# Optimization experiments

Hardware: AMD Instinct MI355X
Metric: run time of the kernel (lower is better)

Reference implementation:

```python
import jax, jax.numpy as jnp
import numpy as np

N = 49152       # nodes
EH = 8192       # hyperedges (star nodes)
M = N + EH
F = 256         # num_features == expan_dim == MLP_hidden
D = 256
HEADS = 8
CHUNK = 1024
NE_N = 10 * N   # nnz of N x N sparse mats
NE_M = 10 * M   # nnz of M x M sparse mats


def spmm(row, col, val, X, n):
    # sparse [n, m] (COO) @ dense X [m, d] -> [n, d]
    return jax.ops.segment_sum(val[:, None] * X[col], row, num_segments=n)


def expan_net(x, row, col, val, Ws, bs, n):
    # 2-layer GCN: (A @ (X @ W) + b), ReLU between; dropout is identity in eval.
    h = spmm(row, col, val, x @ Ws[0], n) + bs[0]
    h = jax.nn.relu(h)
    return spmm(row, col, val, h @ Ws[1], n) + bs[1]


def chunked_mha(q, k, v, in_w, in_b, out_w, out_b):
    # torch nn.MultiheadAttention on unbatched [L, D] chunks of size CHUNK
    n, d = q.shape
    c = n // CHUNK
    dh = d // HEADS
    wq, wk, wv = jnp.split(in_w, 3, axis=0)
    bq, bk, bv = jnp.split(in_b, 3)
    def resh(t):
        return t.reshape(c, CHUNK, HEADS, dh)
    qh = resh(q @ wq.T + bq)
    kh = resh(k @ wk.T + bk)
    vh = resh(v @ wv.T + bv)
    scale = 1.0 / np.sqrt(dh)
    scores = jnp.einsum('clhe,cmhe->chlm', qh, kh) * scale  # [c,H,CHUNK,CHUNK]
    attn = jax.nn.softmax(scores, axis=-1)
    out = jnp.einsum('chlm,cmhe->clhe', attn, vh).reshape(n, d)
    return out @ out_w.T + out_b


def setup_inputs():
    key = jax.random.key(0)
    ks = iter(jax.random.split(key, 64))
    nrm = lambda shape, s=1.0: jax.random.normal(next(ks), shape, dtype=jnp.float32) * s
    uni = lambda shape: jax.random.uniform(next(ks), shape, dtype=jnp.float32)
    ridx = lambda shape, hi: jax.random.randint(next(ks), shape, 0, hi, dtype=jnp.int32)
    inp = {'x': nrm((N, F))}
    for nm, ne, hi in [('A_cg', NE_N, N), ('A_hyp', NE_N, N), ('A_sg', NE_M, M),
                       ('L_cg', NE_N, N), ('L_hyp', NE_N, N), ('L_sg', NE_M, M)]:
        inp[nm + '_row'] = ridx((ne,), hi)
        inp[nm + '_col'] = ridx((ne,), hi)
        inp[nm + '_val'] = uni((ne,)) * 0.1
    for p in ['cg', 'hg', 'sg']:
        inp[p + '_W'] = nrm((2, F, D), 0.05)
        inp[p + '_b'] = nrm((2, D), 0.05)
    for p in ['sn_hyp', 'sn_cg', 'sn_sg']:
        inp[p + '_W'] = nrm((D, D), 0.05)
        inp[p + '_b'] = nrm((D,), 0.05)
    for p in ['spa', 'spe']:
        for q in ['hyp', 'star', 'clq']:
            inp[f'{p}_{q}_W'] = nrm((D, D), 0.05)
            inp[f'{p}_{q}_b'] = nrm((D,), 0.05)
        inp[p + '_in_w'] = nrm((3 * D, D), 0.05)
        inp[p + '_in_b'] = nrm((3 * D,), 0.05)
        inp[p + '_out_w'] = nrm((D, D), 0.05)
        inp[p + '_out_b'] = nrm((D,), 0.05)
    return inp


def reference(x,
              A_cg_row, A_cg_col, A_cg_val, A_hyp_row, A_hyp_col, A_hyp_val,
              A_sg_row, A_sg_col, A_sg_val, L_cg_row, L_cg_col, L_cg_val,
              L_hyp_row, L_hyp_col, L_hyp_val, L_sg_row, L_sg_col, L_sg_val,
              cg_W, cg_b, hg_W, hg_b, sg_W, sg_b,
              sn_hyp_W, sn_hyp_b, sn_cg_W, sn_cg_b, sn_sg_W, sn_sg_b,
              spa_hyp_W, spa_hyp_b, spa_star_W, spa_star_b, spa_clq_W, spa_clq_b,
              spa_in_w, spa_in_b, spa_out_w, spa_out_b,
              spe_hyp_W, spe_hyp_b, spe_star_W, spe_star_b, spe_clq_W, spe_clq_b,
              spe_in_w, spe_in_b, spe_out_w, spe_out_b):
    n = x.shape[0]
    # star features: nodes first, zero-init hyperedge rows (v_mask == [True]*N+[False]*EH)
    x_star = jnp.concatenate([x, jnp.zeros((EH, x.shape[1]), x.dtype)], axis=0)
    # 1. Expansion graph convolutions
    cg_feat = expan_net(x, A_cg_row, A_cg_col, A_cg_val, cg_W, cg_b, n)
    hg_feat = expan_net(x, A_hyp_row, A_hyp_col, A_hyp_val, hg_W, hg_b, n)
    sg_feat = expan_net(x_star, A_sg_row, A_sg_col, A_sg_val, sg_W, sg_b, n + EH)
    X_star, S_star = sg_feat[:n], sg_feat[n:]
    # 2. SmoothNet: linear then Laplacian spmm
    X_hyp = spmm(L_hyp_row, L_hyp_col, L_hyp_val, hg_feat @ sn_hyp_W.T + sn_hyp_b, n)
    X_cg = spmm(L_cg_row, L_cg_col, L_cg_val, cg_feat @ sn_cg_W.T + sn_cg_b, n)
    X_sg = spmm(L_sg_row, L_sg_col, L_sg_val, sg_feat @ sn_sg_W.T + sn_sg_b, n + EH)
    # 3. TAA attention (chunked MHA, Q/K/V = hyp/star/clique projections)
    X_spectral = chunked_mha(X_hyp @ spe_hyp_W.T + spe_hyp_b,
                             X_cg @ spe_star_W.T + spe_star_b,
                             X_sg[:n] @ spe_clq_W.T + spe_clq_b,
                             spe_in_w, spe_in_b, spe_out_w, spe_out_b)
    X_spatial = chunked_mha(hg_feat @ spa_hyp_W.T + spa_hyp_b,
                            cg_feat @ spa_star_W.T + spa_star_b,
                            X_star @ spa_clq_W.T + spa_clq_b,
                            spa_in_w, spa_in_b, spa_out_w, spa_out_b)
    taa = jnp.concatenate([X_spatial, X_spectral], axis=1)
    return taa, X_star, S_star
```

## Files before the change

kernel.cpp:

```cpp
#include <hip/hip_runtime.h>

#define NN 49152
#define EHN 8192
#define MM (NN + EHN)
#define FD 256
#define DD 256
#define NHEADS 8
#define DHEAD 32
#define CHK 1024
#define NEN (10 * NN)
#define NEM (10 * MM)
#define ROWS_TOT (4 * NN + 2 * MM)
#define ETOT (4 * NEN + 2 * NEM)

typedef __bf16 bf16x8 __attribute__((ext_vector_type(8)));
typedef unsigned short u16x8 __attribute__((ext_vector_type(8)));
typedef float f32x4 __attribute__((ext_vector_type(4)));

static __device__ __forceinline__ unsigned short f2bf(float f) {
  unsigned int u = __float_as_uint(f);
  unsigned int r = (u + 0x7FFFu + ((u >> 16) & 1u)) >> 16;
  return (unsigned short)r;
}
static __device__ __forceinline__ float bf2f(unsigned short u) {
  return __uint_as_float((unsigned int)u << 16);
}
static __device__ __forceinline__ unsigned int cvtpk(float a, float b) {
  unsigned int r;
  asm("v_cvt_pk_bf16_f32 %0, %1, %2" : "=v"(r) : "v"(a), "v"(b));
  return r;
}
static __device__ __forceinline__ float max3f(float a, float b, float c) {
  return fmaxf(fmaxf(a, b), c);
}

struct CastJobs {
  const float* src[8];
  unsigned short* dst[8];
  int trans[8];
};
__global__ __launch_bounds__(256) void cast_w8_kernel(CastJobs jobs)
{
  int job = blockIdx.x >> 8;
  int i = (blockIdx.x & 255) * 256 + threadIdx.x;
  int n = i >> 8, k = i & 255;
  const float* src = jobs.src[job];
  float f = jobs.trans[job] ? src[(size_t)k * 256 + n] : src[i];
  jobs.dst[job][i] = f2bf(f);
}

__global__ __launch_bounds__(256) void combine_w_kernel(
    const float* __restrict__ Bw, const float* __restrict__ Aw,
    const float* __restrict__ ab, const float* __restrict__ bb,
    unsigned short* __restrict__ Wc, float* __restrict__ bc, float fscale)
{
  int n = blockIdx.x, t = threadIdx.x;
  __shared__ float shB[256];
  __shared__ float red[256];
  shB[t] = Bw[n * 256 + t];
  __syncthreads();
  float acc = 0.0f;
  #pragma unroll 8
  for (int j = 0; j < 256; ++j) acc += shB[j] * Aw[j * 256 + t];
  Wc[n * 256 + t] = f2bf(acc * fscale);
  red[t] = shB[t] * ab[t];
  __syncthreads();
  for (int off = 128; off; off >>= 1) {
    if (t < off) red[t] += red[t + off];
    __syncthreads();
  }
  if (t == 0) bc[n] = (red[0] + bb[n]) * fscale;
}

__global__ __launch_bounds__(256) void mm256f_kernel(
    const float* __restrict__ A, const float* __restrict__ B,
    float* __restrict__ C)
{
  int n = blockIdx.x, t = threadIdx.x;
  __shared__ float sa[256];
  sa[t] = A[n * 256 + t];
  __syncthreads();
  float acc = 0.0f;
  #pragma unroll 8
  for (int j = 0; j < 256; ++j) acc += sa[j] * B[j * 256 + t];
  C[n * 256 + t] = acc;
}

__global__ __launch_bounds__(256) void mm256b_kernel(
    const float* __restrict__ A, const float* __restrict__ B,
    unsigned short* __restrict__ W, float fs)
{
  int n = blockIdx.x, t = threadIdx.x;
  __shared__ float sa[256];
  sa[t] = A[n * 256 + t];
  __syncthreads();
  float acc = 0.0f;
  #pragma unroll 8
  for (int j = 0; j < 256; ++j) acc += sa[j] * B[j * 256 + t];
  W[n * 256 + t] = f2bf(acc * fs);
}

__global__ __launch_bounds__(256) void mv256_kernel(
    const float* __restrict__ W, const float* __restrict__ v,
    const float* __restrict__ add, float* __restrict__ outv, float fs)
{
  int t = threadIdx.x;
  __shared__ float sv[256];
  sv[t] = v[t];
  __syncthreads();
  float acc = 0.0f;
  #pragma unroll 8
  for (int k = 0; k < 256; ++k) acc += W[t * 256 + k] * sv[k];
  if (add) acc += add[t];
  outv[t] = fs * acc;
}

struct Gemm3 {
  const void* A[3];
  const unsigned short* W[3];
  const float* c0[3];
  const float* rs[3];
  const float* cvec[3];
  unsigned short* out[3];
  int bs1, bs2, btot;
};
template<int ABF>
__global__ __launch_bounds__(256) void gemm3_kernel(Gemm3 g)
{
  const int b = blockIdx.x;
  const int j = (b >= g.bs2) ? 2 : (b >= g.bs1 ? 1 : 0);
  const int bm = (b - (j == 2 ? g.bs2 : j == 1 ? g.bs1 : 0)) * 64;
  const void* Ain = g.A[j];
  const unsigned short* Wt = g.W[j];

  __shared__ __align__(16) char sA[2][4096];
  __shared__ __align__(16) char sB[2][16384];
  const int tid = threadIdx.x, lane = tid & 63, wid = tid >> 6;
  const int l15 = lane & 15, l4 = lane >> 4;

  f32x4 acc[16] = {};
  const int ar = tid >> 2, akq = (tid & 3) * 8;
  const int bn = tid;

  float4 fa0, fa1;
  u16x8 ua;
  u16x8 rb0, rb1, rb2, rb3;
  auto stage_load = [&](int k0) {
    if (ABF) {
      ua = *(const u16x8*)((const unsigned short*)Ain +
                           (size_t)(bm + ar) * 256 + k0 + akq);
    } else {
      const float* ap = (const float*)Ain + (size_t)(bm + ar) * 256 + k0 + akq;
      fa0 = *(const float4*)ap;
      fa1 = *(const float4*)(ap + 4);
    }
    const unsigned short* bp = Wt + (size_t)bn * 256 + k0;
    rb0 = *(const u16x8*)bp;        rb1 = *(const u16x8*)(bp + 8);
    rb2 = *(const u16x8*)(bp + 16); rb3 = *(const u16x8*)(bp + 24);
  };
  auto stage_write = [&](int buf) {
    u16x8 va;
    if (ABF) {
      va = ua;
    } else {
      va[0] = f2bf(fa0.x); va[1] = f2bf(fa0.y); va[2] = f2bf(fa0.z); va[3] = f2bf(fa0.w);
      va[4] = f2bf(fa1.x); va[5] = f2bf(fa1.y); va[6] = f2bf(fa1.z); va[7] = f2bf(fa1.w);
    }
    int aa = ((ar << 6) + (akq << 1)) ^ ((ar & 7) << 4);
    *(u16x8*)(sA[buf] + aa) = va;
    int bb = (bn << 6) ^ ((bn & 7) << 4);
    *(u16x8*)(sB[buf] + bb) = rb0;
    *(u16x8*)(sB[buf] + (bb ^ 16)) = rb1;
    *(u16x8*)(sB[buf] + (bb ^ 32)) = rb2;
    *(u16x8*)(sB[buf] + (bb ^ 48)) = rb3;
  };

  stage_load(0);
  stage_write(0);
  __syncthreads();
  int cur = 0;
  for (int it = 0; it < 8; ++it) {
    if (it < 7) stage_load((it + 1) * 32);
    int ra = wid * 16 + l15;
    bf16x8 af = *(const bf16x8*)(sA[cur] + ((ra << 6) + (l4 << 4) ^ ((ra & 7) << 4)));
    #pragma unroll
    for (int n4 = 0; n4 < 16; ++n4) {
      int rn = n4 * 16 + l15;
      bf16x8 bf = *(const bf16x8*)(sB[cur] + ((rn << 6) + (l4 << 4) ^ ((rn & 7) << 4)));
      acc[n4] = __builtin_amdgcn_mfma_f32_16x16x32_bf16(af, bf, acc[n4], 0, 0, 0);
    }
    __syncthreads();
    if (it < 7) {
      stage_write(cur ^ 1);
      __syncthreads();
      cur ^= 1;
    }
  }
  const int row = bm + wid * 16 + l4 * 4;
  const float* rs = g.rs[j];
  const float* c0 = g.c0[j];
  const float* cvec = g.cvec[j];
  unsigned short* Cout = g.out[j];
  float rsv[4];
  if (rs) {
    #pragma unroll
    for (int jj = 0; jj < 4; ++jj) rsv[jj] = rs[row + jj];
  }
  #pragma unroll
  for (int n4 = 0; n4 < 16; ++n4) {
    int col = n4 * 16 + l15;
    float base = c0 ? c0[col] : 0.0f;
    float cv = rs ? cvec[col] : 0.0f;
    #pragma unroll
    for (int jj = 0; jj < 4; ++jj) {
      float v = acc[n4][jj] + base;
      if (rs) v += rsv[jj] * cv;
      Cout[(size_t)(row + jj) * 256 + col] = f2bf(v);
    }
  }
}

__global__ __launch_bounds__(256) void gemmout2_kernel(
    const unsigned short* __restrict__ A0, const unsigned short* __restrict__ W0,
    const float* __restrict__ b0,
    const unsigned short* __restrict__ A1, const unsigned short* __restrict__ W1,
    const float* __restrict__ b1,
    float* __restrict__ Cout)
{
  const int job = blockIdx.x >= (NN / 64);
  const int bm = (blockIdx.x - (job ? NN / 64 : 0)) * 64;
  const unsigned short* Ain = job ? A1 : A0;
  const unsigned short* Wt  = job ? W1 : W0;
  const float* c0 = job ? b1 : b0;
  const int coff = job ? 0 : 256;

  __shared__ __align__(16) char sA[2][4096];
  __shared__ __align__(16) char sB[2][16384];
  const int tid = threadIdx.x, lane = tid & 63, wid = tid >> 6;
  const int l15 = lane & 15, l4 = lane >> 4;

  f32x4 acc[16] = {};
  const int ar = tid >> 2, akq = (tid & 3) * 8;
  const int bn = tid;
  u16x8 ua, rb0, rb1, rb2, rb3;
  auto stage_load = [&](int k0) {
    ua = *(const u16x8*)(Ain + (size_t)(bm + ar) * 256 + k0 + akq);
    const unsigned short* bp = Wt + (size_t)bn * 256 + k0;
    rb0 = *(const u16x8*)bp;        rb1 = *(const u16x8*)(bp + 8);
    rb2 = *(const u16x8*)(bp + 16); rb3 = *(const u16x8*)(bp + 24);
  };
  auto stage_write = [&](int buf) {
    int aa = ((ar << 6) + (akq << 1)) ^ ((ar & 7) << 4);
    *(u16x8*)(sA[buf] + aa) = ua;
    int bb = (bn << 6) ^ ((bn & 7) << 4);
    *(u16x8*)(sB[buf] + bb) = rb0;
    *(u16x8*)(sB[buf] + (bb ^ 16)) = rb1;
    *(u16x8*)(sB[buf] + (bb ^ 32)) = rb2;
    *(u16x8*)(sB[buf] + (bb ^ 48)) = rb3;
  };
  stage_load(0);
  stage_write(0);
  __syncthreads();
  int cur = 0;
  for (int it = 0; it < 8; ++it) {
    if (it < 7) stage_load((it + 1) * 32);
    int ra = wid * 16 + l15;
    bf16x8 af = *(const bf16x8*)(sA[cur] + ((ra << 6) + (l4 << 4) ^ ((ra & 7) << 4)));
    #pragma unroll
    for (int n4 = 0; n4 < 16; ++n4) {
      int rn = n4 * 16 + l15;
      bf16x8 bf = *(const bf16x8*)(sB[cur] + ((rn << 6) + (l4 << 4) ^ ((rn & 7) << 4)));
      acc[n4] = __builtin_amdgcn_mfma_f32_16x16x32_bf16(af, bf, acc[n4], 0, 0, 0);
    }
    __syncthreads();
    if (it < 7) {
      stage_write(cur ^ 1);
      __syncthreads();
      cur ^= 1;
    }
  }
  const int row = bm + wid * 16 + l4 * 4;
  #pragma unroll
  for (int n4 = 0; n4 < 16; ++n4) {
    int col = n4 * 16 + l15;
    float base = c0[col];
    #pragma unroll
    for (int jj = 0; jj < 4; ++jj)
      Cout[(size_t)(row + jj) * 512 + coff + col] = acc[n4][jj] + base;
  }
}

struct CooPtrs {
  const int* rw[6];
  const int* cl[6];
  const float* vl[6];
};
static __device__ __forceinline__ void coo_block_resolve(
    int b, int& g, int& eb, int& rb)
{
  if      (b < 1920) { g = 0; eb = 0;    rb = 0; }
  else if (b < 3840) { g = 1; eb = 1920; rb = NN; }
  else if (b < 6080) { g = 2; eb = 3840; rb = 2 * NN; }
  else if (b < 8000) { g = 3; eb = 6080; rb = 2 * NN + MM; }
  else if (b < 9920) { g = 4; eb = 8000; rb = 3 * NN + MM; }
  else               { g = 5; eb = 9920; rb = 4 * NN + MM; }
}

__global__ __launch_bounds__(256) void count_all_kernel(
    CooPtrs coo, int* __restrict__ cnt)
{
  int g, eb, rb;
  coo_block_resolve(blockIdx.x, g, eb, rb);
  int e = (blockIdx.x - eb) * 256 + threadIdx.x;
  atomicAdd(&cnt[rb + coo.rw[g][e]], 1);
}

__global__ __launch_bounds__(256) void scan1_kernel(
    const int* __restrict__ cnt, int* __restrict__ bsum, int n)
{
  __shared__ int sh[256];
  int i = blockIdx.x * 256 + threadIdx.x;
  sh[threadIdx.x] = (i < n) ? cnt[i] : 0;
  __syncthreads();
  for (int off = 128; off; off >>= 1) {
    if (threadIdx.x < off) sh[threadIdx.x] += sh[threadIdx.x + off];
    __syncthreads();
  }
  if (threadIdx.x == 0) bsum[blockIdx.x] = sh[0];
}

__global__ __launch_bounds__(256) void scan2_kernel(int* __restrict__ bsum, int nb)
{
  __shared__ int sh[256];
  int t = threadIdx.x;
  int carry = 0;
  for (int base = 0; base < nb; base += 256) {
    int i = base + t;
    int v = (i < nb) ? bsum[i] : 0;
    sh[t] = v;
    __syncthreads();
    for (int off = 1; off < 256; off <<= 1) {
      int add = (t >= off) ? sh[t - off] : 0;
      __syncthreads();
      sh[t] += add;
      __syncthreads();
    }
    int incl = sh[t];
    int tot = sh[255];
    if (i < nb) bsum[i] = carry + incl - v;
    carry += tot;
    __syncthreads();
  }
}

__global__ __launch_bounds__(256) void scan3_kernel(
    const int* __restrict__ cnt, const int* __restrict__ bsum,
    int* __restrict__ rowptr, int* __restrict__ cntz, int n)
{
  __shared__ int sh[256];
  int i = blockIdx.x * 256 + threadIdx.x;
  int v = (i < n) ? cnt[i] : 0;
  sh[threadIdx.x] = v;
  __syncthreads();
  for (int off = 1; off < 256; off <<= 1) {
    int add = (threadIdx.x >= off) ? sh[threadIdx.x - off] : 0;
    __syncthreads();
    sh[threadIdx.x] += add;
    __syncthreads();
  }
  int incl = sh[threadIdx.x];
  int base = bsum[blockIdx.x];
  if (i < n) { rowptr[i] = base + incl - v; cntz[i] = 0; }
  if (i == n - 1) rowptr[n] = base + incl;
}

__global__ __launch_bounds__(256) void fill_all_kernel(
    CooPtrs coo, const int* __restrict__ P, int* __restrict__ cur,
    int2* __restrict__ epack)
{
  int g, eb, rb;
  coo_block_resolve(blockIdx.x, g, eb, rb);
  int e = (blockIdx.x - eb) * 256 + threadIdx.x;
  int grow = rb + coo.rw[g][e];
  int pos = P[grow] + atomicAdd(&cur[grow], 1);
  epack[pos] = make_int2(coo.cl[g][e], __float_as_int(coo.vl[g][e]));
}

__global__ __launch_bounds__(256) void rowsum_all_kernel(
    const int* __restrict__ P, const int2* __restrict__ epack,
    float* __restrict__ rsAll)
{
  int j = blockIdx.x * 256 + threadIdx.x;
  int g = j / NN;
  int r = j - g * NN;
  int grow = (g == 0 ? 2 * NN + MM : g == 1 ? 3 * NN + MM : 4 * NN + MM) + r;
  float s = 0.0f;
  int end = P[grow + 1];
  for (int e = P[grow]; e < end; ++e) s += __int_as_float(epack[e].y);
  rsAll[j] = s;
}

struct Spmm3 {
  const int* rowptr[3];
  const unsigned short* X[3];
  unsigned short* Y[3];
  float* Y2[3];
  const float* bias[3];
  int src_rows[3];
  int bs1, bs2;
};
__global__ __launch_bounds__(256) void spmm3_kernel(
    Spmm3 s, const int2* __restrict__ ep, int relu)
{
  const int b = blockIdx.x;
  const int j = (b >= s.bs2) ? 2 : (b >= s.bs1 ? 1 : 0);
  const int rblk = b - (j == 2 ? s.bs2 : j == 1 ? s.bs1 : 0);
  const int wave = threadIdx.x >> 6, lane = threadIdx.x & 63;
  const int r = rblk * 4 + wave;
  const int f0 = lane * 4;
  const int src_rows = s.src_rows[j];
  const unsigned short* X = s.X[j];
  const int* rowptr = s.rowptr[j];
  int e = rowptr[r], end = rowptr[r + 1];
  float a0 = 0.0f, a1 = 0.0f, a2 = 0.0f, a3 = 0.0f;
  for (; e + 3 < end; e += 4) {
    int2 cv0 = ep[e], cv1 = ep[e + 1], cv2 = ep[e + 2], cv3 = ep[e + 3];
    ushort4 x0 = {0,0,0,0}, x1 = {0,0,0,0}, x2 = {0,0,0,0}, x3 = {0,0,0,0};
    if (cv0.x < src_rows) x0 = *(const ushort4*)(X + (size_t)cv0.x * DD + f0);
    if (cv1.x < src_rows) x1 = *(const ushort4*)(X + (size_t)cv1.x * DD + f0);
    if (cv2.x < src_rows) x2 = *(const ushort4*)(X + (size_t)cv2.x * DD + f0);
    if (cv3.x < src_rows) x3 = *(const ushort4*)(X + (size_t)cv3.x * DD + f0);
    float v0 = __int_as_float(cv0.y), v1 = __int_as_float(cv1.y);
    float v2 = __int_as_float(cv2.y), v3 = __int_as_float(cv3.y);
    if (cv0.x < src_rows) { a0 += v0*bf2f(x0.x); a1 += v0*bf2f(x0.y); a2 += v0*bf2f(x0.z); a3 += v0*bf2f(x0.w); }
    if (cv1.x < src_rows) { a0 += v1*bf2f(x1.x); a1 += v1*bf2f(x1.y); a2 += v1*bf2f(x1.z); a3 += v1*bf2f(x1.w); }
    if (cv2.x < src_rows) { a0 += v2*bf2f(x2.x); a1 += v2*bf2f(x2.y); a2 += v2*bf2f(x2.z); a3 += v2*bf2f(x2.w); }
    if (cv3.x < src_rows) { a0 += v3*bf2f(x3.x); a1 += v3*bf2f(x3.y); a2 += v3*bf2f(x3.z); a3 += v3*bf2f(x3.w); }
  }
  for (; e < end; ++e) {
    int2 cv = ep[e];
    if (cv.x < src_rows) {
      float v = __int_as_float(cv.y);
      ushort4 xx = *(const ushort4*)(X + (size_t)cv.x * DD + f0);
      a0 += v * bf2f(xx.x); a1 += v * bf2f(xx.y);
      a2 += v * bf2f(xx.z); a3 += v * bf2f(xx.w);
    }
  }
  const float* bias = s.bias[j];
  if (bias) {
    a0 += bias[f0]; a1 += bias[f0 + 1]; a2 += bias[f0 + 2]; a3 += bias[f0 + 3];
  }
  if (relu) {
    a0 = fmaxf(a0, 0.0f); a1 = fmaxf(a1, 0.0f);
    a2 = fmaxf(a2, 0.0f); a3 = fmaxf(a3, 0.0f);
  }
  uint2 yb = { cvtpk(a0, a1), cvtpk(a2, a3) };
  *(uint2*)(s.Y[j] + (size_t)r * DD + f0) = yb;
  if (s.Y2[j]) {
    float4 yf = {a0, a1, a2, a3};
    *(float4*)(s.Y2[j] + (size_t)r * DD + f0) = yf;
  }
}

__global__ __launch_bounds__(256) void attn2_kernel(
    const unsigned short* __restrict__ Q1, const unsigned short* __restrict__ K1,
    const unsigned short* __restrict__ V1, unsigned short* __restrict__ O1,
    const unsigned short* __restrict__ Q2, const unsigned short* __restrict__ K2,
    const unsigned short* __restrict__ V2, unsigned short* __restrict__ O2)
{
  __shared__ __align__(16) char sKb[4096];
  __shared__ __align__(16) char sVb[4096];
  __shared__ __align__(16) char sPb[8192];
  const int wgid = (blockIdx.x & 7) * 1536 + (blockIdx.x >> 3);
  const int qb = wgid & 15, h = (wgid >> 4) & 7, cc = wgid >> 7;
  const int job = cc >= 48;
  const int c = cc - (job ? 48 : 0);
  const unsigned short* Q = job ? Q2 : Q1;
  const unsigned short* K = job ? K2 : K1;
  const unsigned short* V = job ? V2 : V1;
  unsigned short* O = job ? O2 : O1;

  const int tid = threadIdx.x, lane = tid & 63, wid = tid >> 6;
  const int l15 = lane & 15, l4 = lane >> 4;
  char* sPw = sPb + wid * 2048;
  const size_t base = (size_t)c * (CHK * DD) + (size_t)h * DHEAD;
  const int q0 = qb * 64 + wid * 16;

  bf16x8 qf = *(const bf16x8*)(Q + base + (size_t)(q0 + l15) * DD + l4 * 8);

  const int key_s = tid >> 2, dq = (tid & 3) * 8;
  const unsigned short* Kp = K + base + (size_t)key_s * DD + dq;
  const unsigned short* Vp = V + base + (size_t)key_s * DD + dq;
  const int kaddr = ((key_s << 6) + (dq << 1)) ^ ((key_s & 7) << 4);

  f32x4 oacc[2] = {};
  float m = -1e30f, l = 0.0f;
  const f32x4 zero = {};

  for (int kt = 0; kt < CHK; kt += 64) {
    __syncthreads();
    u16x8 kv = *(const u16x8*)Kp;  Kp += 64 * DD;
    u16x8 vv = *(const u16x8*)Vp;  Vp += 64 * DD;
    *(u16x8*)(sKb + kaddr) = kv;
    #pragma unroll
    for (int i = 0; i < 8; ++i) {
      int d = dq + i;
      int bb = ((d << 7) + (key_s << 1))
             ^ ((d & 7) << 4) ^ (((d >> 3) & 3) << 5);
      *(unsigned short*)(sVb + bb) = vv[i];
    }
    __syncthreads();

    f32x4 s[4];
    #pragma unroll
    for (int s4 = 0; s4 < 4; ++s4) {
      int key = s4 * 16 + l15;
      int ba = ((key << 6) + (l4 << 4)) ^ ((key & 7) << 4);
      bf16x8 kf = *(const bf16x8*)(sKb + ba);
      s[s4] = __builtin_amdgcn_mfma_f32_16x16x32_bf16(kf, qf, zero, 0, 0, 0);
    }
    float t0 = max3f(s[0][0], s[0][1], s[0][2]);
    float t1 = max3f(s[0][3], s[1][0], s[1][1]);
    float t2 = max3f(s[1][2], s[1][3], s[2][0]);
    float t3 = max3f(s[2][1], s[2][2], s[2][3]);
    float t4 = max3f(s[3][0], s[3][1], s[3][2]);
    float tmax = max3f(max3f(t0, t1, t2), fmaxf(t3, t4), s[3][3]);
    tmax = fmaxf(tmax, __shfl_xor(tmax, 16));
    tmax = fmaxf(tmax, __shfl_xor(tmax, 32));
    bool skip = __all(tmax - m <= 8.0f);
    float mnew = skip ? m : fmaxf(m, tmax);
    if (!skip) {
      float corr = __builtin_amdgcn_exp2f(m - mnew);
      l *= corr;
      oacc[0] *= corr;
      oacc[1] *= corr;
    }
    float psum = 0.0f;
    float p[4][4];
    #pragma unroll
    for (int s4 = 0; s4 < 4; ++s4)
      #pragma unroll
      for (int j = 0; j < 4; ++j) {
        p[s4][j] = __builtin_amdgcn_exp2f(s[s4][j] - mnew);
        psum += p[s4][j];
      }
    psum += __shfl_xor(psum, 16);
    psum += __shfl_xor(psum, 32);
    l += psum;
    m = mnew;
    #pragma unroll
    for (int s4 = 0; s4 < 4; ++s4) {
      uint2 pk = { cvtpk(p[s4][0], p[s4][1]), cvtpk(p[s4][2], p[s4][3]) };
      int bp = ((l15 << 7) + (s4 << 5) + (l4 << 3)) ^ ((l15 & 3) << 5);
      *(uint2*)(sPw + bp) = pk;
    }
    __syncthreads();

    #pragma unroll
    for (int dh = 0; dh < 2; ++dh)
      #pragma unroll
      for (int kh = 0; kh < 2; ++kh) {
        int d = dh * 16 + l15;
        int ba = ((d << 7) + ((kh * 32 + l4 * 8) << 1))
               ^ ((d & 7) << 4) ^ (((d >> 3) & 3) << 5);
        bf16x8 vf = *(const bf16x8*)(sVb + ba);
        int bp = ((l15 << 7) + (kh << 6) + (l4 << 4)) ^ ((l15 & 3) << 5);
        bf16x8 pf = *(const bf16x8*)(sPw + bp);
        oacc[dh] = __builtin_amdgcn_mfma_f32_16x16x32_bf16(vf, pf, oacc[dh], 0, 0, 0);
      }
  }

  float inv = 1.0f / l;
  unsigned short* orow = O + base + (size_t)(q0 + l15) * DD;
  #pragma unroll
  for (int dh = 0; dh < 2; ++dh) {
    uint2 o2 = { cvtpk(oacc[dh][0] * inv, oacc[dh][1] * inv),
                 cvtpk(oacc[dh][2] * inv, oacc[dh][3] * inv) };
    *(uint2*)(orow + dh * 16 + l4 * 4) = o2;
  }
}

__global__ __launch_bounds__(256) void fill_kernel(float* p, long n, float v)
{
  long i = (long)blockIdx.x * 256 + threadIdx.x;
  if (i < n) p[i] = v;
}

extern "C" void kernel_launch(void* const* d_in, const int* in_sizes, int n_in,
                              void* d_out, int out_size, void* d_ws, size_t ws_size,
                              hipStream_t stream)
{
  const float* x     = (const float*)d_in[0];
  const int*   Acg_r = (const int*)d_in[1];
  const int*   Acg_c = (const int*)d_in[2];
  const float* Acg_v = (const float*)d_in[3];
  const int*   Ahy_r = (const int*)d_in[4];
  const int*   Ahy_c = (const int*)d_in[5];
  const float* Ahy_v = (const float*)d_in[6];
  const int*   Asg_r = (const int*)d_in[7];
  const int*   Asg_c = (const int*)d_in[8];
  const float* Asg_v = (const float*)d_in[9];
  const int*   Lcg_r = (const int*)d_in[10];
  const int*   Lcg_c = (const int*)d_in[11];
  const float* Lcg_v = (const float*)d_in[12];
  const int*   Lhy_r = (const int*)d_in[13];
  const int*   Lhy_c = (const int*)d_in[14];
  const float* Lhy_v = (const float*)d_in[15];
  const int*   Lsg_r = (const int*)d_in[16];
  const int*   Lsg_c = (const int*)d_in[17];
  const float* Lsg_v = (const float*)d_in[18];
  const float* cg_W  = (const float*)d_in[19];
  const float* cg_b  = (const float*)d_in[20];
  const float* hg_W  = (const float*)d_in[21];
  const float* hg_b  = (const float*)d_in[22];
  const float* sg_W  = (const float*)d_in[23];
  const float* sg_b  = (const float*)d_in[24];
  const float* snh_W = (const float*)d_in[25];
  const float* snh_b = (const float*)d_in[26];
  const float* snc_W = (const float*)d_in[27];
  const float* snc_b = (const float*)d_in[28];
  const float* sns_W = (const float*)d_in[29];
  const float* sns_b = (const float*)d_in[30];
  const float* spa_hyp_W  = (const float*)d_in[31];
  const float* spa_hyp_b  = (const float*)d_in[32];
  const float* spa_star_W = (const float*)d_in[33];
  const float* spa_star_b = (const float*)d_in[34];
  const float* spa_clq_W  = (const float*)d_in[35];
  const float* spa_clq_b  = (const float*)d_in[36];
  const float* spa_in_w   = (const float*)d_in[37];
  const float* spa_in_b   = (const float*)d_in[38];
  const float* spa_out_w  = (const float*)d_in[39];
  const float* spa_out_b  = (const float*)d_in[40];
  const float* spe_hyp_W  = (const float*)d_in[41];
  const float* spe_hyp_b  = (const float*)d_in[42];
  const float* spe_star_W = (const float*)d_in[43];
  const float* spe_star_b = (const float*)d_in[44];
  const float* spe_clq_W  = (const float*)d_in[45];
  const float* spe_clq_b  = (const float*)d_in[46];
  const float* spe_in_w   = (const float*)d_in[47];
  const float* spe_in_b   = (const float*)d_in[48];
  const float* spe_out_w  = (const float*)d_in[49];
  const float* spe_out_b  = (const float*)d_in[50];

  float* out = (float*)d_out;

  const size_t NF = (size_t)NN * DD;
  const size_t MF = (size_t)MM * DD;
  const size_t WELEMS  = 14u * 65536u;
  const size_t need = (14 * NF + 3 * MF) * 2
                    + (size_t)ETOT * 8
                    + ((size_t)3 * NN + 65536 + 256 + 4096) * 4
                    + ((size_t)ROWS_TOT + 1 + ROWS_TOT + 2048) * 4
                    + WELEMS * 2;

  auto fill = [&](float v) {
    long tot = (long)out_size;
    fill_kernel<<<dim3((unsigned)((tot + 255) / 256)), 256, 0, stream>>>(out, tot, v);
  };
  if (ws_size < need)                        { fill(12.0f); return; }
  if (n_in != 51)                            { fill(16.0f); return; }
  if (in_sizes[0] != NN * FD)                { fill(20.0f); return; }
  if (in_sizes[3] != NEN)                    { fill(24.0f); return; }
  if (in_sizes[9] != NEM)                    { fill(28.0f); return; }
  if (in_sizes[19] != 2 * FD * DD)           { fill(32.0f); return; }
  if (in_sizes[37] != 3 * DD * DD)           { fill(36.0f); return; }
  if (out_size != NN * 512 + NN * DD + EHN * DD) { fill(40.0f); return; }

  unsigned short* Tcg = (unsigned short*)d_ws;
  unsigned short* Thy = Tcg + NF;
  unsigned short* Tsg = Thy + NF;
  unsigned short* Hcg = Tsg + NF;
  unsigned short* Hhy = Hcg + NF;
  unsigned short* Hsg = Hhy + NF;
  unsigned short* Usg = Hsg + MF;
  unsigned short* SG  = Usg + MF;
  unsigned short* CG  = SG + MF;
  unsigned short* HG  = CG + NF;
  unsigned short* LH  = HG + NF;
  unsigned short* LC  = LH + NF;
  unsigned short* LS  = LC + NF;
  unsigned short* QH  = LS + NF;
  unsigned short* KH  = QH + NF;
  unsigned short* VH  = KH + NF;
  unsigned short* AOx = VH + NF;
  unsigned short* Ucg = Tcg;
  unsigned short* Uhy = Thy;
  unsigned short* Q2  = LH;
  unsigned short* K2  = LC;
  unsigned short* V2  = LS;
  unsigned short* AO1 = Hcg;
  unsigned short* AO2 = Hhy;
  (void)AOx;

  int2* epack = (int2*)(AOx + NF);
  float* fp = (float*)(epack + ETOT);
  float* rsAll = fp;           fp += 3 * NN;
  float* tmp256 = fp;          fp += 65536;
  float* tmpv = fp;            fp += 256;
  float* CB = fp;              fp += 4096;
  int* P    = (int*)fp;
  int* cnt  = P + ROWS_TOT + 1;
  int* bsum = cnt + ROWS_TOT;
  unsigned short* WB = (unsigned short*)(bsum + 2048);

  int* rp_cg  = P;
  int* rp_hy  = P + NN;
  int* rp_sg  = P + 2 * NN;
  int* rp_Lcg = P + 2 * NN + MM;
  int* rp_Lhy = P + 3 * NN + MM;
  int* rp_Lsg = P + 4 * NN + MM;
  float* rs_c = rsAll;
  float* rs_h = rsAll + NN;
  float* rs_s = rsAll + 2 * NN;

  auto wslot = [&](int s) { return WB + (size_t)s * 65536; };
  auto cb    = [&](int s) { return CB + (size_t)s * 256; };

  auto combine = [&](const float* Bw, const float* Aw, const float* ab,
                     const float* bb, unsigned short* Wc, float* bcp, float fs) {
    combine_w_kernel<<<dim3(256), 256, 0, stream>>>(Bw, Aw, ab, bb, Wc, bcp, fs);
  };
  auto combine3 = [&](const float* w3, const float* b3, const float* pW,
                      const float* pb, const float* sW, const float* sb,
                      unsigned short* Wc, float* cvecp, float* c0p, float fs) {
    mm256f_kernel<<<dim3(256), 256, 0, stream>>>(pW, sW, tmp256);
    mm256b_kernel<<<dim3(256), 256, 0, stream>>>(w3, tmp256, Wc, fs);
    mv256_kernel<<<dim3(1), 256, 0, stream>>>(pW, sb, nullptr, tmpv, 1.0f);
    mv256_kernel<<<dim3(1), 256, 0, stream>>>(w3, tmpv, nullptr, cvecp, fs);
    mv256_kernel<<<dim3(1), 256, 0, stream>>>(w3, pb, b3, c0p, fs);
  };

  const float fsQ = 0.17677669529663687f * 1.4426950408889634f;

  {
    CastJobs jobs;
    jobs.src[0] = cg_W;           jobs.dst[0] = wslot(0);  jobs.trans[0] = 1;
    jobs.src[1] = cg_W + FD * DD; jobs.dst[1] = wslot(1);  jobs.trans[1] = 1;
    jobs.src[2] = hg_W;           jobs.dst[2] = wslot(2);  jobs.trans[2] = 1;
    jobs.src[3] = hg_W + FD * DD; jobs.dst[3] = wslot(3);  jobs.trans[3] = 1;
    jobs.src[4] = sg_W;           jobs.dst[4] = wslot(4);  jobs.trans[4] = 1;
    jobs.src[5] = sg_W + FD * DD; jobs.dst[5] = wslot(5);  jobs.trans[5] = 1;
    jobs.src[6] = spa_out_w;      jobs.dst[6] = wslot(12); jobs.trans[6] = 0;
    jobs.src[7] = spe_out_w;      jobs.dst[7] = wslot(13); jobs.trans[7] = 0;
    cast_w8_kernel<<<dim3(8 * 256), 256, 0, stream>>>(jobs);
  }
  combine(spa_in_w,                spa_hyp_W,  spa_hyp_b,  spa_in_b,          wslot(6), cb(0), fsQ);
  combine(spa_in_w + DD * DD,      spa_star_W, spa_star_b, spa_in_b + DD,     wslot(7), cb(1), 1.0f);
  combine(spa_in_w + 2 * DD * DD,  spa_clq_W,  spa_clq_b,  spa_in_b + 2 * DD, wslot(8), cb(2), 1.0f);
  combine3(spe_in_w,               spe_in_b,            spe_hyp_W,  spe_hyp_b,  snh_W, snh_b, wslot(9),  cb(3), cb(4), fsQ);
  combine3(spe_in_w + DD * DD,     spe_in_b + DD,       spe_star_W, spe_star_b, snc_W, snc_b, wslot(10), cb(5), cb(6), 1.0f);
  combine3(spe_in_w + 2 * DD * DD, spe_in_b + 2 * DD,   spe_clq_W,  spe_clq_b,  sns_W, sns_b, wslot(11), cb(7), cb(8), 1.0f);

  {
    CooPtrs coo;
    coo.rw[0] = Acg_r; coo.cl[0] = Acg_c; coo.vl[0] = Acg_v;
    coo.rw[1] = Ahy_r; coo.cl[1] = Ahy_c; coo.vl[1] = Ahy_v;
    coo.rw[2] = Asg_r; coo.cl[2] = Asg_c; coo.vl[2] = Asg_v;
    coo.rw[3] = Lcg_r; coo.cl[3] = Lcg_c; coo.vl[3] = Lcg_v;
    coo.rw[4] = Lhy_r; coo.cl[4] = Lhy_c; coo.vl[4] = Lhy_v;
    coo.rw[5] = Lsg_r; coo.cl[5] = Lsg_c; coo.vl[5] = Lsg_v;
    hipMemsetAsync(cnt, 0, (size_t)ROWS_TOT * 4, stream);
    count_all_kernel<<<dim3(ETOT / 256), 256, 0, stream>>>(coo, cnt);
    scan1_kernel<<<dim3(ROWS_TOT / 256), 256, 0, stream>>>(cnt, bsum, ROWS_TOT);
    scan2_kernel<<<dim3(1), 256, 0, stream>>>(bsum, ROWS_TOT / 256);
    scan3_kernel<<<dim3(ROWS_TOT / 256), 256, 0, stream>>>(cnt, bsum, P, cnt, ROWS_TOT);
    fill_all_kernel<<<dim3(ETOT / 256), 256, 0, stream>>>(coo, P, cnt, epack);
    rowsum_all_kernel<<<dim3(3 * NN / 256), 256, 0, stream>>>(P, epack, rsAll);
  }

  {
    Gemm3 g = {};
    for (int j = 0; j < 3; ++j) { g.A[j] = x; g.c0[j] = nullptr; g.rs[j] = nullptr; }
    g.W[0] = wslot(0); g.out[0] = Tcg;
    g.W[1] = wslot(2); g.out[1] = Thy;
    g.W[2] = wslot(4); g.out[2] = Tsg;
    g.bs1 = 768; g.bs2 = 1536; g.btot = 2304;
    gemm3_kernel<0><<<dim3(2304), 256, 0, stream>>>(g);
  }
  {
    Spmm3 s = {};
    s.rowptr[0] = rp_cg; s.X[0] = Tcg; s.Y[0] = Hcg; s.Y2[0] = nullptr; s.bias[0] = cg_b; s.src_rows[0] = NN;
    s.rowptr[1] = rp_hy; s.X[1] = Thy; s.Y[1] = Hhy; s.Y2[1] = nullptr; s.bias[1] = hg_b; s.src_rows[1] = NN;
    s.rowptr[2] = rp_sg; s.X[2] = Tsg; s.Y[2] = Hsg; s.Y2[2] = nullptr; s.bias[2] = sg_b; s.src_rows[2] = NN;
    s.bs1 = NN / 4; s.bs2 = 2 * (NN / 4);
    spmm3_kernel<<<dim3(2 * (NN / 4) + MM / 4), 256, 0, stream>>>(s, epack, 1);
  }
  {
    Gemm3 g = {};
    g.A[0] = Hcg; g.W[0] = wslot(1); g.out[0] = Ucg;
    g.A[1] = Hhy; g.W[1] = wslot(3); g.out[1] = Uhy;
    g.A[2] = Hsg; g.W[2] = wslot(5); g.out[2] = Usg;
    for (int j = 0; j < 3; ++j) { g.c0[j] = nullptr; g.rs[j] = nullptr; }
    g.bs1 = NN / 64; g.bs2 = 2 * (NN / 64); g.btot = 2 * (NN / 64) + MM / 64;
    gemm3_kernel<1><<<dim3(2 * (NN / 64) + MM / 64), 256, 0, stream>>>(g);
  }
  {
    Spmm3 s = {};
    s.rowptr[0] = rp_cg; s.X[0] = Ucg; s.Y[0] = CG; s.Y2[0] = nullptr; s.bias[0] = cg_b + DD; s.src_rows[0] = NN;
    s.rowptr[1] = rp_hy; s.X[1] = Uhy; s.Y[1] = HG; s.Y2[1] = nullptr; s.bias[1] = hg_b + DD; s.src_rows[1] = NN;
    s.rowptr[2] = rp_sg; s.X[2] = Usg; s.Y[2] = SG; s.Y2[2] = out + (size_t)NN * 512; s.bias[2] = sg_b + DD; s.src_rows[2] = MM;
    s.bs1 = NN / 4; s.bs2 = 2 * (NN / 4);
    spmm3_kernel<<<dim3(2 * (NN / 4) + MM / 4), 256, 0, stream>>>(s, epack, 0);
  }
  {
    Spmm3 s = {};
    s.rowptr[0] = rp_Lhy; s.X[0] = HG; s.Y[0] = LH; s.Y2[0] = nullptr; s.bias[0] = nullptr; s.src_rows[0] = NN;
    s.rowptr[1] = rp_Lcg; s.X[1] = CG; s.Y[1] = LC; s.Y2[1] = nullptr; s.bias[1] = nullptr; s.src_rows[1] = NN;
    s.rowptr[2] = rp_Lsg; s.X[2] = SG; s.Y[2] = LS; s.Y2[2] = nullptr; s.bias[2] = nullptr; s.src_rows[2] = MM;
    s.bs1 = NN / 4; s.bs2 = 2 * (NN / 4);
    spmm3_kernel<<<dim3(3 * (NN / 4)), 256, 0, stream>>>(s, epack, 0);
  }

  {
    Gemm3 g = {};
    g.A[0] = LH; g.W[0] = wslot(9);  g.c0[0] = cb(4); g.rs[0] = rs_h; g.cvec[0] = cb(3); g.out[0] = QH;
    g.A[1] = LC; g.W[1] = wslot(10); g.c0[1] = cb(6); g.rs[1] = rs_c; g.cvec[1] = cb(5); g.out[1] = KH;
    g.A[2] = LS; g.W[2] = wslot(11); g.c0[2] = cb(8); g.rs[2] = rs_s; g.cvec[2] = cb(7); g.out[2] = VH;
    g.bs1 = 768; g.bs2 = 1536; g.btot = 2304;
    gemm3_kernel<1><<<dim3(2304), 256, 0, stream>>>(g);
  }
  {
    Gemm3 g = {};
    g.A[0] = HG; g.W[0] = wslot(6); g.c0[0] = cb(0); g.rs[0] = nullptr; g.out[0] = Q2;
    g.A[1] = CG; g.W[1] = wslot(7); g.c0[1] = cb(1); g.rs[1] = nullptr; g.out[1] = K2;
    g.A[2] = SG; g.W[2] = wslot(8); g.c0[2] = cb(2); g.rs[2] = nullptr; g.out[2] = V2;
    g.bs1 = 768; g.bs2 = 1536; g.btot = 2304;
    gemm3_kernel<1><<<dim3(2304), 256, 0, stream>>>(g);
  }
  attn2_kernel<<<dim3(12288), 256, 0, stream>>>(QH, KH, VH, AO1,
                                                Q2, K2, V2, AO2);
  gemmout2_kernel<<<dim3(2 * (NN / 64)), 256, 0, stream>>>(
      AO1, wslot(13), spe_out_b,
      AO2, wslot(12), spa_out_b,
      out);
}
```

Baseline: 1.632 ms.

## Fuse six projection GEMMs into one launch and enlarge attention key tiles

Merges the two three-way projection GEMM launches into a single six-job kernel. Their outputs are redirected to separate scratch buffers (Tcg/Thy/Tsg), because the spatial Q/K/V previously reused the LH/LC/LS buffers, which are now still being read in the same launch. The attention kernel now processes 128-key tiles instead of 64, prefetches the next K/V tile into registers before the current compute, and drops a block barrier that was unnecessary since each wave owns its own P buffer. This cuts launch count and barrier/loop overhead, at the cost of doubled shared memory and more registers in attention.

```diff
diff --git a/kernel.cpp b/kernel.cpp
--- a/kernel.cpp
+++ b/kernel.cpp
@@ -220,19 +220,20 @@
   }
 }
 
-__global__ __launch_bounds__(256) void gemmout2_kernel(
-    const unsigned short* __restrict__ A0, const unsigned short* __restrict__ W0,
-    const float* __restrict__ b0,
-    const unsigned short* __restrict__ A1, const unsigned short* __restrict__ W1,
-    const float* __restrict__ b1,
-    float* __restrict__ Cout)
-{
-  const int job = blockIdx.x >= (NN / 64);
-  const int bm = (blockIdx.x - (job ? NN / 64 : 0)) * 64;
-  const unsigned short* Ain = job ? A1 : A0;
-  const unsigned short* Wt  = job ? W1 : W0;
-  const float* c0 = job ? b1 : b0;
-  const int coff = job ? 0 : 256;
+struct Gemm6 {
+  const unsigned short* A[6];
+  const unsigned short* W[6];
+  const float* c0[6];
+  const float* rs[6];
+  const float* cvec[6];
+  unsigned short* out[6];
+};
+__global__ __launch_bounds__(256) void gemm6_kernel(Gemm6 g)
+{
+  const int j = blockIdx.x / (NN / 64);
+  const int bm = (blockIdx.x - j * (NN / 64)) * 64;
+  const unsigned short* Ain = g.A[j];
+  const unsigned short* Wt = g.W[j];
 
   __shared__ __align__(16) char sA[2][4096];
   __shared__ __align__(16) char sB[2][16384];
@@ -280,6 +281,89 @@
     }
   }
   const int row = bm + wid * 16 + l4 * 4;
+  const float* rs = g.rs[j];
+  const float* c0 = g.c0[j];
+  const float* cvec = g.cvec[j];
+  unsigned short* Cout = g.out[j];
+  float rsv[4];
+  if (rs) {
+    #pragma unroll
+    for (int jj = 0; jj < 4; ++jj) rsv[jj] = rs[row + jj];
+  }
+  #pragma unroll
+  for (int n4 = 0; n4 < 16; ++n4) {
+    int col = n4 * 16 + l15;
+    float base = c0[col];
+    float cv = rs ? cvec[col] : 0.0f;
+    #pragma unroll
+    for (int jj = 0; jj < 4; ++jj) {
+      float v = acc[n4][jj] + base;
+      if (rs) v += rsv[jj] * cv;
+      Cout[(size_t)(row + jj) * 256 + col] = f2bf(v);
+    }
+  }
+}
+
+__global__ __launch_bounds__(256) void gemmout2_kernel(
+    const unsigned short* __restrict__ A0, const unsigned short* __restrict__ W0,
+    const float* __restrict__ b0,
+    const unsigned short* __restrict__ A1, const unsigned short* __restrict__ W1,
+    const float* __restrict__ b1,
+    float* __restrict__ Cout)
+{
+  const int job = blockIdx.x >= (NN / 64);
+  const int bm = (blockIdx.x - (job ? NN / 64 : 0)) * 64;
+  const unsigned short* Ain = job ? A1 : A0;
+  const unsigned short* Wt  = job ? W1 : W0;
+  const float* c0 = job ? b1 : b0;
+  const int coff = job ? 0 : 256;
+
+  __shared__ __align__(16) char sA[2][4096];
+  __shared__ __align__(16) char sB[2][16384];
+  const int tid = threadIdx.x, lane = tid & 63, wid = tid >> 6;
+  const int l15 = lane & 15, l4 = lane >> 4;
+
+  f32x4 acc[16] = {};
+  const int ar = tid >> 2, akq = (tid & 3) * 8;
+  const int bn = tid;
+  u16x8 ua, rb0, rb1, rb2, rb3;
+  auto stage_load = [&](int k0) {
+    ua = *(const u16x8*)(Ain + (size_t)(bm + ar) * 256 + k0 + akq);
+    const unsigned short* bp = Wt + (size_t)bn * 256 + k0;
+    rb0 = *(const u16x8*)bp;        rb1 = *(const u16x8*)(bp + 8);
+    rb2 = *(const u16x8*)(bp + 16); rb3 = *(const u16x8*)(bp + 24);
+  };
+  auto stage_write = [&](int buf) {
+    int aa = ((ar << 6) + (akq << 1)) ^ ((ar & 7) << 4);
+    *(u16x8*)(sA[buf] + aa) = ua;
+    int bb = (bn << 6) ^ ((bn & 7) << 4);
+    *(u16x8*)(sB[buf] + bb) = rb0;
+    *(u16x8*)(sB[buf] + (bb ^ 16)) = rb1;
+    *(u16x8*)(sB[buf] + (bb ^ 32)) = rb2;
+    *(u16x8*)(sB[buf] + (bb ^ 48)) = rb3;
+  };
+  stage_load(0);
+  stage_write(0);
+  __syncthreads();
+  int cur = 0;
+  for (int it = 0; it < 8; ++it) {
+    if (it < 7) stage_load((it + 1) * 32);
+    int ra = wid * 16 + l15;
+    bf16x8 af = *(const bf16x8*)(sA[cur] + ((ra << 6) + (l4 << 4) ^ ((ra & 7) << 4)));
+    #pragma unroll
+    for (int n4 = 0; n4 < 16; ++n4) {
+      int rn = n4 * 16 + l15;
+      bf16x8 bf = *(const bf16x8*)(sB[cur] + ((rn << 6) + (l4 << 4) ^ ((rn & 7) << 4)));
+      acc[n4] = __builtin_amdgcn_mfma_f32_16x16x32_bf16(af, bf, acc[n4], 0, 0, 0);
+    }
+    __syncthreads();
+    if (it < 7) {
+      stage_write(cur ^ 1);
+      __syncthreads();
+      cur ^= 1;
+    }
+  }
+  const int row = bm + wid * 16 + l4 * 4;
   #pragma unroll
   for (int n4 = 0; n4 < 16; ++n4) {
     int col = n4 * 16 + l15;
@@ -468,9 +552,9 @@
     const unsigned short* __restrict__ Q2, const unsigned short* __restrict__ K2,
     const unsigned short* __restrict__ V2, unsigned short* __restrict__ O2)
 {
-  __shared__ __align__(16) char sKb[4096];
-  __shared__ __align__(16) char sVb[4096];
-  __shared__ __align__(16) char sPb[8192];
+  __shared__ __align__(16) char sKb[8192];
+  __shared__ __align__(16) char sVb[8192];
+  __shared__ __align__(16) char sPb[16384];
   const int wgid = (blockIdx.x & 7) * 1536 + (blockIdx.x >> 3);
   const int qb = wgid & 15, h = (wgid >> 4) & 7, cc = wgid >> 7;
   const int job = cc >= 48;
@@ -482,7 +566,7 @@
 
   const int tid = threadIdx.x, lane = tid & 63, wid = tid >> 6;
   const int l15 = lane & 15, l4 = lane >> 4;
-  char* sPw = sPb + wid * 2048;
+  char* sPw = sPb + wid * 4096;
   const size_t base = (size_t)c * (CHK * DD) + (size_t)h * DHEAD;
   const int q0 = qb * 64 + wid * 16;
 
@@ -497,34 +581,47 @@
   float m = -1e30f, l = 0.0f;
   const f32x4 zero = {};
 
-  for (int kt = 0; kt < CHK; kt += 64) {
-    __syncthreads();
-    u16x8 kv = *(const u16x8*)Kp;  Kp += 64 * DD;
-    u16x8 vv = *(const u16x8*)Vp;  Vp += 64 * DD;
-    *(u16x8*)(sKb + kaddr) = kv;
+  u16x8 kv0 = *(const u16x8*)Kp;
+  u16x8 kv1 = *(const u16x8*)(Kp + 64 * DD);
+  u16x8 vv0 = *(const u16x8*)Vp;
+  u16x8 vv1 = *(const u16x8*)(Vp + 64 * DD);
+  Kp += 128 * DD;  Vp += 128 * DD;
+
+  for (int kt = 0; kt < CHK; kt += 128) {
+    __syncthreads();
+    *(u16x8*)(sKb + kaddr) = kv0;
+    *(u16x8*)(sKb + kaddr + 4096) = kv1;
     #pragma unroll
     for (int i = 0; i < 8; ++i) {
       int d = dq + i;
-      int bb = ((d << 7) + (key_s << 1))
+      int bb = ((d << 8) + (key_s << 1))
              ^ ((d & 7) << 4) ^ (((d >> 3) & 3) << 5);
-      *(unsigned short*)(sVb + bb) = vv[i];
-    }
-    __syncthreads();
-
-    f32x4 s[4];
-    #pragma unroll
-    for (int s4 = 0; s4 < 4; ++s4) {
+      *(unsigned short*)(sVb + bb) = vv0[i];
+      *(unsigned short*)(sVb + bb + 128) = vv1[i];
+    }
+    __syncthreads();
+    if (kt + 128 < CHK) {
+      kv0 = *(const u16x8*)Kp;
+      kv1 = *(const u16x8*)(Kp + 64 * DD);
+      vv0 = *(const u16x8*)Vp;
+      vv1 = *(const u16x8*)(Vp + 64 * DD);
+      Kp += 128 * DD;  Vp += 128 * DD;
+    }
+
+    f32x4 s[8];
+    #pragma unroll
+    for (int s4 = 0; s4 < 8; ++s4) {
       int key = s4 * 16 + l15;
       int ba = ((key << 6) + (l4 << 4)) ^ ((key & 7) << 4);
       bf16x8 kf = *(const bf16x8*)(sKb + ba);
       s[s4] = __builtin_amdgcn_mfma_f32_16x16x32_bf16(kf, qf, zero, 0, 0, 0);
     }
-    float t0 = max3f(s[0][0], s[0][1], s[0][2]);
-    float t1 = max3f(s[0][3], s[1][0], s[1][1]);
-    float t2 = max3f(s[1][2], s[1][3], s[2][0]);
-    float t3 = max3f(s[2][1], s[2][2], s[2][3]);
-    float t4 = max3f(s[3][0], s[3][1], s[3][2]);
-    float tmax = max3f(max3f(t0, t1, t2), fmaxf(t3, t4), s[3][3]);
+    float u[8];
+    #pragma unroll
+    for (int s4 = 0; s4 < 8; ++s4)
+      u[s4] = fmaxf(fmaxf(s[s4][0], s[s4][1]), fmaxf(s[s4][2], s[s4][3]));
+    float tmax = max3f(max3f(u[0], u[1], u[2]), max3f(u[3], u[4], u[5]),
+                       fmaxf(u[6], u[7]));
     tmax = fmaxf(tmax, __shfl_xor(tmax, 16));
     tmax = fmaxf(tmax, __shfl_xor(tmax, 32));
     bool skip = __all(tmax - m <= 8.0f);
@@ -536,9 +633,9 @@
       oacc[1] *= corr;
     }
     float psum = 0.0f;
-    float p[4][4];
-    #pragma unroll
-    for (int s4 = 0; s4 < 4; ++s4)
+    float p[8][4];
+    #pragma unroll
+    for (int s4 = 0; s4 < 8; ++s4)
       #pragma unroll
       for (int j = 0; j < 4; ++j) {
         p[s4][j] = __builtin_amdgcn_exp2f(s[s4][j] - mnew);
@@ -549,22 +646,21 @@
     l += psum;
     m = mnew;
     #pragma unroll
-    for (int s4 = 0; s4 < 4; ++s4) {
+    for (int s4 = 0; s4 < 8; ++s4) {
       uint2 pk = { cvtpk(p[s4][0], p[s4][1]), cvtpk(p[s4][2], p[s4][3]) };
-      int bp = ((l15 << 7) + (s4 << 5) + (l4 << 3)) ^ ((l15 & 3) << 5);
+      int bp = ((l15 << 8) + (s4 << 5) + (l4 << 3)) ^ ((l15 & 7) << 4);
       *(uint2*)(sPw + bp) = pk;
     }
-    __syncthreads();
 
     #pragma unroll
     for (int dh = 0; dh < 2; ++dh)
       #pragma unroll
-      for (int kh = 0; kh < 2; ++kh) {
+      for (int kh = 0; kh < 4; ++kh) {
         int d = dh * 16 + l15;
-        int ba = ((d << 7) + ((kh * 32 + l4 * 8) << 1))
+        int ba = ((d << 8) + ((kh * 32 + l4 * 8) << 1))
                ^ ((d & 7) << 4) ^ (((d >> 3) & 3) << 5);
         bf16x8 vf = *(const bf16x8*)(sVb + ba);
-        int bp = ((l15 << 7) + (kh << 6) + (l4 << 4)) ^ ((l15 & 3) << 5);
+        int bp = ((l15 << 8) + (kh << 6) + (l4 << 4)) ^ ((l15 & 7) << 4);
         bf16x8 pf = *(const bf16x8*)(sPw + bp);
         oacc[dh] = __builtin_amdgcn_mfma_f32_16x16x32_bf16(vf, pf, oacc[dh], 0, 0, 0);
       }
@@ -685,9 +781,9 @@
   unsigned short* AOx = VH + NF;
   unsigned short* Ucg = Tcg;
   unsigned short* Uhy = Thy;
-  unsigned short* Q2  = LH;
-  unsigned short* K2  = LC;
-  unsigned short* V2  = LS;
+  unsigned short* Q2  = Tcg;
+  unsigned short* K2  = Thy;
+  unsigned short* V2  = Tsg;
   unsigned short* AO1 = Hcg;
   unsigned short* AO2 = Hhy;
   (void)AOx;
@@ -812,20 +908,14 @@
   }
 
   {
-    Gemm3 g = {};
-    g.A[0] = LH; g.W[0] = wslot(9);  g.c0[0] = cb(4); g.rs[0] = rs_h; g.cvec[0] = cb(3); g.out[0] = QH;
-    g.A[1] = LC; g.W[1] = wslot(10); g.c0[1] = cb(6); g.rs[1] = rs_c; g.cvec[1] = cb(5); g.out[1] = KH;
-    g.A[2] = LS; g.W[2] = wslot(11); g.c0[2] = cb(8); g.rs[2] = rs_s; g.cvec[2] = cb(7); g.out[2] = VH;
-    g.bs1 = 768; g.bs2 = 1536; g.btot = 2304;
-    gemm3_kernel<1><<<dim3(2304), 256, 0, stream>>>(g);
-  }
-  {
-    Gemm3 g = {};
-    g.A[0] = HG; g.W[0] = wslot(6); g.c0[0] = cb(0); g.rs[0] = nullptr; g.out[0] = Q2;
-    g.A[1] = CG; g.W[1] = wslot(7); g.c0[1] = cb(1); g.rs[1] = nullptr; g.out[1] = K2;
-    g.A[2] = SG; g.W[2] = wslot(8); g.c0[2] = cb(2); g.rs[2] = nullptr; g.out[2] = V2;
-    g.bs1 = 768; g.bs2 = 1536; g.btot = 2304;
-    gemm3_kernel<1><<<dim3(2304), 256, 0, stream>>>(g);
+    Gemm6 g;
+    g.A[0] = LH; g.W[0] = wslot(9);  g.c0[0] = cb(4); g.rs[0] = rs_h;   g.cvec[0] = cb(3);   g.out[0] = QH;
+    g.A[1] = LC; g.W[1] = wslot(10); g.c0[1] = cb(6); g.rs[1] = rs_c;   g.cvec[1] = cb(5);   g.out[1] = KH;
+    g.A[2] = LS; g.W[2] = wslot(11); g.c0[2] = cb(8); g.rs[2] = rs_s;   g.cvec[2] = cb(7);   g.out[2] = VH;
+    g.A[3] = HG; g.W[3] = wslot(6);  g.c0[3] = cb(0); g.rs[3] = nullptr; g.cvec[3] = nullptr; g.out[3] = Q2;
+    g.A[4] = CG; g.W[4] = wslot(7);  g.c0[4] = cb(1); g.rs[4] = nullptr; g.cvec[4] = nullptr; g.out[4] = K2;
+    g.A[5] = SG; g.W[5] = wslot(8);  g.c0[5] = cb(2); g.rs[5] = nullptr; g.cvec[5] = nullptr; g.out[5] = V2;
+    gemm6_kernel<<<dim3(6 * (NN / 64)), 256, 0, stream>>>(g);
   }
   attn2_kernel<<<dim3(12288), 256, 0, stream>>>(QH, KH, VH, AO1,
                                                 Q2, K2, V2, AO2);
```

Result: faster. 1.586 ms (-2.9%).
